# Kernel tuning notes

Measured on AMD Instinct MI355X. Metric: run time of the kernel, lower is better.

The kernel has to match this reference:

```python
import math
import jax, jax.numpy as jnp
import numpy as np

B, S, T, C, H = 4, 100, 128, 256, 256
NH, DH = 4, 32            # num_attention_heads//2, hidden_size//num_attention_heads
AH = NH * DH              # all_head_size = 128
FH = 32                   # fire_hidden_size
MAX_SP, MAX_TM, MAX_DOY = 180.0, 365.0, 182.0


def _fire(dist, c, w1, w2, max_dist):
    # FIREDistanceBias: log-compressed distance -> MLP(1->FH, SiLU, FH->1, no bias)
    c = jnp.maximum(c, 0.0)
    d = jnp.log(c * dist + 1.0) / jnp.log(c * max_dist + 1.0)
    h = jax.nn.silu(d[..., None] * w1[:, 0])   # (..., FH)
    return h @ w2[0]                            # (...,)


def setup_inputs() -> dict:
    key = jax.random.key(0)
    ks = jax.random.split(key, 20)
    p = 0.02
    inp = {
        "hidden_states": jax.random.normal(ks[0], (B, S, T, H), jnp.float32),
        "source_embeddings": jax.random.normal(ks[1], (B, S, C, H), jnp.float32),
        "attention_mask": jnp.zeros((B, 1, 1, T, C), jnp.float32),
        "st_dist": jax.random.uniform(ks[2], (B, T, C, 2), jnp.float32)
                   * jnp.array([MAX_SP, MAX_TM], jnp.float32),
        "st_doy_dist": jax.random.uniform(ks[3], (B, T, C), jnp.float32) * MAX_DOY,
        # attention projections (Linear H->AH with bias), output dense (AH->H)
        "Wq": jax.random.normal(ks[4], (AH, H), jnp.float32) * p,
        "bq": jnp.zeros((AH,), jnp.float32),
        "Wk": jax.random.normal(ks[5], (AH, H), jnp.float32) * p,
        "bk": jnp.zeros((AH,), jnp.float32),
        "Wv": jax.random.normal(ks[6], (AH, H), jnp.float32) * p,
        "bv": jnp.zeros((AH,), jnp.float32),
        "Wo": jax.random.normal(ks[7], (H, AH), jnp.float32) * p,
        "bo": jnp.zeros((H,), jnp.float32),
        # FIRE params: spatial / temporal / seasonal
        "c_s": jnp.float32(100.0),
        "w1_s": jax.random.normal(ks[8], (FH, 1), jnp.float32) * 0.5,
        "w2_s": jax.random.normal(ks[9], (1, FH), jnp.float32) * 0.5,
        "c_t": jnp.float32(100.0),
        "w1_t": jax.random.normal(ks[10], (FH, 1), jnp.float32) * 0.5,
        "w2_t": jax.random.normal(ks[11], (1, FH), jnp.float32) * 0.5,
        "c_d": jnp.float32(100.0),
        "w1_d": jax.random.normal(ks[12], (FH, 1), jnp.float32) * 0.5,
        "w2_d": jax.random.normal(ks[13], (1, FH), jnp.float32) * 0.5,
        # per-species log scales (init zeros in torch)
        "s_log_scale": jnp.zeros((S,), jnp.float32),
        "t_log_scale": jnp.zeros((S,), jnp.float32),
    }
    return inp


def reference(hidden_states, source_embeddings, attention_mask, st_dist, st_doy_dist,
              Wq, bq, Wk, bk, Wv, bv, Wo, bo,
              c_s, w1_s, w2_s, c_t, w1_t, w2_t, c_d, w1_d, w2_d,
              s_log_scale, t_log_scale):
    # FIRE distance biases over (B, T, C)
    sb = _fire(st_dist[..., 0], c_s, w1_s, w2_s, MAX_SP)
    tb = _fire(st_dist[..., 1], c_t, w1_t, w2_t, MAX_TM)
    db = _fire(st_doy_dist, c_d, w1_d, w2_d, MAX_DOY)
    # (B, S, T, C): species-scaled spatial+temporal + seasonal bias
    bias = (sb[:, None] * jnp.exp(s_log_scale)[None, :, None, None]
            + tb[:, None] * jnp.exp(t_log_scale)[None, :, None, None]
            + db[:, None])

    # projections; split heads: (B,S,L,AH) -> (B,S,NH,L,DH)
    q = (hidden_states @ Wq.T + bq).reshape(B, S, T, NH, DH).transpose(0, 1, 3, 2, 4)
    k = (source_embeddings @ Wk.T + bk).reshape(B, S, C, NH, DH).transpose(0, 1, 3, 2, 4)
    v = (source_embeddings @ Wv.T + bv).reshape(B, S, C, NH, DH).transpose(0, 1, 3, 2, 4)

    scores = jnp.einsum('bshtd,bshcd->bshtc', q, k) / math.sqrt(DH)
    scores = scores + attention_mask + bias[:, :, None]   # mask (B,1,1,T,C), bias (B,S,1,T,C)
    probs = jax.nn.softmax(scores, axis=-1)
    ctx = jnp.einsum('bshtc,bshcd->bshtd', probs, v)
    ctx = ctx.transpose(0, 1, 3, 2, 4).reshape(B, S, T, AH)
    return ctx @ Wo.T + bo   # STCrossOutput dense (dropout=0, eval)
```

## Files before the change

kernel.cpp:

```cpp
#include <hip/hip_runtime.h>
#include <hip/hip_bf16.h>
#include <math.h>

#define Bdim 4
#define Sdim 100
#define Tdim 128
#define Cdim 256
#define Hdim 256
#define NHd  4
#define DHd  32
#define AHd  128

typedef short bf16x8 __attribute__((ext_vector_type(8)));
typedef float f32x4 __attribute__((ext_vector_type(4)));

#define WAITCNT_V(n) do { \
  asm volatile("s_waitcnt vmcnt(" #n ")" ::: "memory"); \
  __builtin_amdgcn_sched_barrier(0); \
} while (0)

__device__ __forceinline__ short f2b(float x) {
  unsigned u = __float_as_uint(x);
  unsigned r = (u + 0x7FFF + ((u >> 16) & 1)) >> 16;
  return (short)r;
}

__device__ __forceinline__ void split2(float x, short& hi, short& lo) {
  unsigned u = __float_as_uint(x) & 0xFFFF0000u;
  hi = (short)(u >> 16);
  lo = f2b(x - __uint_as_float(u));
}

__device__ __forceinline__ float fire_eval(float dist, float c,
                                           const float* __restrict__ w1,
                                           const float* __restrict__ w2,
                                           float maxd) {
  c = fmaxf(c, 0.0f);
  float d = logf(fmaf(c, dist, 1.0f)) / logf(fmaf(c, maxd, 1.0f));
  float acc = 0.0f;
#pragma unroll
  for (int j = 0; j < 32; ++j) {
    float x = d * w1[j];
    float h = x / (1.0f + expf(-x));
    acc = fmaf(h, w2[j], acc);
  }
  return acc;
}

__global__ __launch_bounds__(256) void fire_bias_kernel(
    const float* __restrict__ st_dist, const float* __restrict__ st_doy,
    const float* __restrict__ mask,
    const float* __restrict__ c_s, const float* __restrict__ w1_s, const float* __restrict__ w2_s,
    const float* __restrict__ c_t, const float* __restrict__ w1_t, const float* __restrict__ w2_t,
    const float* __restrict__ c_d, const float* __restrict__ w1_d, const float* __restrict__ w2_d,
    float4* __restrict__ pk) {
  int i = blockIdx.x * 256 + threadIdx.x;
  if (i >= Bdim * Tdim * Cdim) return;
  float2 dv = ((const float2*)st_dist)[i];
  float4 r;
  r.x = fire_eval(dv.x, c_s[0], w1_s, w2_s, 180.0f);
  r.y = fire_eval(dv.y, c_t[0], w1_t, w2_t, 365.0f);
  r.z = fire_eval(st_doy[i], c_d[0], w1_d, w2_d, 182.0f) + mask[i];
  r.w = 0.0f;
  pk[i] = r;
}

__global__ __launch_bounds__(256) void bias_combine(
    const float4* __restrict__ pk,
    const float* __restrict__ sls, const float* __restrict__ tls,
    float* __restrict__ bC) {
  const int b = blockIdx.y;
  const int base = blockIdx.x * 1024 + threadIdx.x * 4;
  const float4* src = pk + (size_t)b * Tdim * Cdim + base;
  float sb[4], tb[4], db[4];
#pragma unroll
  for (int i = 0; i < 4; ++i) {
    float4 v = src[i];
    sb[i] = v.x; tb[i] = v.y; db[i] = v.z;
  }
  float* dst = bC + ((size_t)b * Sdim) * Tdim * Cdim + base;
  for (int s = 0; s < Sdim; ++s) {
    float es = __expf(sls[s]), et = __expf(tls[s]);
    float4 o;
    o.x = fmaf(sb[0], es, fmaf(tb[0], et, db[0]));
    o.y = fmaf(sb[1], es, fmaf(tb[1], et, db[1]));
    o.z = fmaf(sb[2], es, fmaf(tb[2], et, db[2]));
    o.w = fmaf(sb[3], es, fmaf(tb[3], et, db[3]));
    *(float4*)(dst + (size_t)s * Tdim * Cdim) = o;
  }
}

__global__ __launch_bounds__(256) void wsplit_pack(
    const float* __restrict__ Wq, const float* __restrict__ Wk,
    const float* __restrict__ Wv, const float* __restrict__ Wo,
    short* __restrict__ pack) {
  int which = blockIdx.y;
  const float* W = which == 0 ? Wq : which == 1 ? Wk : which == 2 ? Wv : Wo;
  int idx = blockIdx.x * 256 + threadIdx.x;
  int j = idx & 7;
  int l = (idx >> 3) & 63;
  int frag = idx >> 9;
  int nt, kk8, Kd;
  if (which == 3) { nt = frag & 15; kk8 = frag >> 4; Kd = 128; }
  else           { nt = frag & 7;  kk8 = frag >> 3; Kd = 256; }
  int n = nt * 16 + (l & 15);
  int k = kk8 * 32 + (l >> 4) * 8 + j;
  float val = W[(size_t)n * Kd + k];
  short h, lo_;
  if (which == 3) split2(val, h, lo_);
  else { h = f2b(val); lo_ = 0; }
  pack[(size_t)which * 65536 + idx] = h;
  pack[(size_t)which * 65536 + 32768 + idx] = lo_;
}


__global__ __launch_bounds__(512, 4) void proj_q_mfma(
    const float* __restrict__ A, const short* __restrict__ Wp,
    const float* __restrict__ bias, short* __restrict__ O, float scale) {
  __shared__ short wlds[2][8 * 512];
  const int tid = threadIdx.x;
  const int l = tid & 63, w = tid >> 6;
  const int lr = l & 15, lg = l >> 4;
  const int m0 = blockIdx.x * 128;
  const int arow = m0 + w * 16 + lr;
  const float* ap = A + (size_t)arow * 256 + lg * 8;

  auto stage = [&](int buf, int kk) {
    const short* gsrc = Wp + ((size_t)(kk * 8 + w) * 64 + l) * 8;
    int loff = __builtin_amdgcn_readfirstlane(buf * 4096 + w * 512);
    __builtin_amdgcn_global_load_lds(gsrc, &wlds[0][0] + loff, 16, 0, 0);
  };

  f32x4 acc[8] = {};
  stage(0, 0);
  float4 ca = *(const float4*)ap;
  float4 cb = *(const float4*)(ap + 4);
#pragma unroll
  for (int kk = 0; kk < 8; ++kk) {
    const int buf = kk & 1;
    float4 na, nb;
    if (kk < 7) {
      stage(buf ^ 1, kk + 1);
      const float* np = ap + (kk + 1) * 32;
      na = *(const float4*)np;
      nb = *(const float4*)(np + 4);
    }
    float av[8] = {ca.x, ca.y, ca.z, ca.w, cb.x, cb.y, cb.z, cb.w};
    bf16x8 af;
#pragma unroll
    for (int e = 0; e < 8; ++e) af[e] = f2b(av[e]);
    if (kk < 7) { WAITCNT_V(3); } else { WAITCNT_V(0); }
    __builtin_amdgcn_s_barrier();
    const short* lb = &wlds[0][0] + buf * 4096 + l * 8;
#pragma unroll
    for (int nt = 0; nt < 8; ++nt) {
      bf16x8 wv = *(const bf16x8*)(lb + nt * 512);
      acc[nt] = __builtin_amdgcn_mfma_f32_16x16x32_bf16(af, wv, acc[nt], 0, 0, 0);
    }
    __builtin_amdgcn_s_barrier();
    if (kk < 7) { ca = na; cb = nb; }
  }
#pragma unroll
  for (int nt = 0; nt < 8; ++nt)
#pragma unroll
    for (int r = 0; r < 4; ++r)
      O[(size_t)(m0 + w * 16 + lg * 4 + r) * 128 + nt * 16 + lr] =
          f2b((acc[nt][r] + bias[nt * 16 + lr]) * scale);
}

__global__ __launch_bounds__(512, 4) void proj_kv_mfma(
    const float* __restrict__ A,
    const short* __restrict__ Wkp, const float* __restrict__ bk,
    const short* __restrict__ Wvp, const float* __restrict__ bv,
    short* __restrict__ Ko, short* __restrict__ Vo) {
  __shared__ short wlds[2][16 * 512];
  const int tid = threadIdx.x;
  const int l = tid & 63, w = tid >> 6;
  const int lr = l & 15, lg = l >> 4;
  const int m0 = blockIdx.x * 128;
  const int arow = m0 + w * 16 + lr;
  const float* ap = A + (size_t)arow * 256 + lg * 8;

  auto stage = [&](int buf, int kk) {
#pragma unroll
    for (int r = 0; r < 2; ++r) {
      int f = w + 8 * r;
      const short* gsrc = (r ? Wvp : Wkp) + ((size_t)(kk * 8 + w) * 64 + l) * 8;
      int loff = __builtin_amdgcn_readfirstlane(buf * 8192 + f * 512);
      __builtin_amdgcn_global_load_lds(gsrc, &wlds[0][0] + loff, 16, 0, 0);
    }
  };

  f32x4 accK[8] = {}, accV[8] = {};
  stage(0, 0);
  float4 ca = *(const float4*)ap;
  float4 cb = *(const float4*)(ap + 4);
#pragma unroll
  for (int kk = 0; kk < 8; ++kk) {
    const int buf = kk & 1;
    float4 na, nb;
    if (kk < 7) {
      stage(buf ^ 1, kk + 1);
      const float* np = ap + (kk + 1) * 32;
      na = *(const float4*)np;
      nb = *(const float4*)(np + 4);
    }
    float av[8] = {ca.x, ca.y, ca.z, ca.w, cb.x, cb.y, cb.z, cb.w};
    bf16x8 af;
#pragma unroll
    for (int e = 0; e < 8; ++e) af[e] = f2b(av[e]);
    if (kk < 7) { WAITCNT_V(4); } else { WAITCNT_V(0); }
    __builtin_amdgcn_s_barrier();
    const short* lb = &wlds[0][0] + buf * 8192 + l * 8;
#pragma unroll
    for (int nt = 0; nt < 8; ++nt) {
      bf16x8 kw = *(const bf16x8*)(lb + nt * 512);
      bf16x8 vw = *(const bf16x8*)(lb + (8 + nt) * 512);
      accK[nt] = __builtin_amdgcn_mfma_f32_16x16x32_bf16(af, kw, accK[nt], 0, 0, 0);
      accV[nt] = __builtin_amdgcn_mfma_f32_16x16x32_bf16(af, vw, accV[nt], 0, 0, 0);
    }
    __builtin_amdgcn_s_barrier();
    if (kk < 7) { ca = na; cb = nb; }
  }
#pragma unroll
  for (int nt = 0; nt < 8; ++nt)
#pragma unroll
    for (int r = 0; r < 4; ++r) {
      size_t row = (size_t)(m0 + w * 16 + lg * 4 + r) * 128 + nt * 16 + lr;
      Ko[row] = f2b(accK[nt][r] + bk[nt * 16 + lr]);
      Vo[row] = f2b(accV[nt][r] + bv[nt * 16 + lr]);
    }
}

__global__ __launch_bounds__(512, 4) void proj_o_mfma(
    const short* __restrict__ Ahi, const short* __restrict__ Alo,
    const short* __restrict__ Wp, const float* __restrict__ bias,
    float* __restrict__ O) {
  __shared__ short wlds[2][32 * 512];
  const int tid = threadIdx.x;
  const int l = tid & 63, w = tid >> 6;
  const int lr = l & 15, lg = l >> 4;
  const int m0 = blockIdx.x * 128;
  const int arow = m0 + w * 16 + lr;
  const short* ah = Ahi + (size_t)arow * 128 + lg * 8;
  const short* al = Alo + (size_t)arow * 128 + lg * 8;

  auto stage = [&](int buf, int kk) {
#pragma unroll
    for (int r = 0; r < 4; ++r) {
      int f = w + 8 * r;
      const short* gsrc = Wp + ((f >> 4) ? 32768 : 0)
                          + ((size_t)(kk * 16 + (f & 15)) * 64 + l) * 8;
      int loff = __builtin_amdgcn_readfirstlane(buf * 16384 + f * 512);
      __builtin_amdgcn_global_load_lds(gsrc, &wlds[0][0] + loff, 16, 0, 0);
    }
  };

  f32x4 acc[16] = {};
  stage(0, 0);
  bf16x8 cah = *(const bf16x8*)ah;
  bf16x8 cal = *(const bf16x8*)al;
#pragma unroll
  for (int kk = 0; kk < 4; ++kk) {
    const int buf = kk & 1;
    bf16x8 nah, nal;
    if (kk < 3) {
      stage(buf ^ 1, kk + 1);
      nah = *(const bf16x8*)(ah + (kk + 1) * 32);
      nal = *(const bf16x8*)(al + (kk + 1) * 32);
    }
    if (kk < 3) { WAITCNT_V(6); } else { WAITCNT_V(0); }
    __builtin_amdgcn_s_barrier();
    const short* lb = &wlds[0][0] + buf * 16384 + l * 8;
#pragma unroll
    for (int nt = 0; nt < 16; ++nt) {
      bf16x8 whi = *(const bf16x8*)(lb + nt * 512);
      bf16x8 wlo = *(const bf16x8*)(lb + (16 + nt) * 512);
      acc[nt] = __builtin_amdgcn_mfma_f32_16x16x32_bf16(cah, whi, acc[nt], 0, 0, 0);
      acc[nt] = __builtin_amdgcn_mfma_f32_16x16x32_bf16(cah, wlo, acc[nt], 0, 0, 0);
      acc[nt] = __builtin_amdgcn_mfma_f32_16x16x32_bf16(cal, whi, acc[nt], 0, 0, 0);
    }
    __builtin_amdgcn_s_barrier();
    if (kk < 3) { cah = nah; cal = nal; }
  }
#pragma unroll
  for (int nt = 0; nt < 16; ++nt)
#pragma unroll
    for (int r = 0; r < 4; ++r)
      O[(size_t)(m0 + w * 16 + lg * 4 + r) * 256 + nt * 16 + lr] =
          acc[nt][r] + bias[nt * 16 + lr];
}

__global__ __launch_bounds__(512) void attn_mfma(
    const short* __restrict__ Qb, const short* __restrict__ Kb,
    const short* __restrict__ Vb,
    const float* __restrict__ bC,
    short* __restrict__ Chi, short* __restrict__ Clo) {
  __shared__ short vfrag[8][2][64][8];
  __shared__ short pbuf[8][16 * 36];

  const int tid = threadIdx.x;
  const int l = tid & 63;
  const int w = tid >> 6;
  const int lr = l & 15, lg = l >> 4;
  const int bid = blockIdx.x;
  const int xcd = bid & 7;
  const int i_  = bid >> 3;
  const int bs  = xcd * 50 + (i_ >> 2);
  const int h   = i_ & 3;

  const size_t kvbase = (size_t)bs * Cdim * AHd + h * DHd;
  const size_t qbase  = (size_t)bs * Tdim * AHd + h * DHd;

#pragma unroll
  for (int rep = 0; rep < 2; ++rep) {
    int chunk = tid * 2 + rep;
    int c = chunk >> 2, q = chunk & 3;
    bf16x8 v8 = *(const bf16x8*)(Vb + kvbase + (size_t)c * AHd + q * 8);
    int kc = c >> 5, nt = q >> 1;
    int lanebase = ((c & 31) >> 3) * 16 + (q & 1) * 8;
    int j = c & 7;
#pragma unroll
    for (int e = 0; e < 8; ++e)
      vfrag[kc][nt][lanebase + e][j] = v8[e];
  }
  __syncthreads();

  bf16x8 qf = *(const bf16x8*)(Qb + qbase + (size_t)(w * 16 + lr) * AHd + lg * 8);
  bf16x8 kf[16];
#pragma unroll
  for (int nt = 0; nt < 16; ++nt)
    kf[nt] = *(const bf16x8*)(Kb + kvbase + (size_t)(nt * 16 + lr) * AHd + lg * 8);

  const float* bb = bC + (size_t)bs * Tdim * Cdim + (size_t)(w * 16) * Cdim;
  f32x4 sacc[16];
#pragma unroll
  for (int nt = 0; nt < 16; ++nt) {
    f32x4 cinit;
#pragma unroll
    for (int r = 0; r < 4; ++r)
      cinit[r] = bb[(size_t)(lg * 4 + r) * Cdim + nt * 16 + lr];
    sacc[nt] = __builtin_amdgcn_mfma_f32_16x16x32_bf16(qf, kf[nt], cinit, 0, 0, 0);
  }

  float rinv[4];
#pragma unroll
  for (int nt = 0; nt < 16; ++nt)
#pragma unroll
    for (int r = 0; r < 4; ++r)
      sacc[nt][r] = __expf(sacc[nt][r]);
#pragma unroll
  for (int r = 0; r < 4; ++r) {
    float su = 0.f;
#pragma unroll
    for (int nt = 0; nt < 16; ++nt) su += sacc[nt][r];
#pragma unroll
    for (int off = 1; off < 16; off <<= 1) su += __shfl_xor(su, off);
    rinv[r] = 1.0f / su;
  }

  const f32x4 zero = {0.f, 0.f, 0.f, 0.f};
  f32x4 cacc[2] = {zero, zero};
  short* pb = &pbuf[w][0];
#pragma unroll
  for (int kc = 0; kc < 8; ++kc) {
#pragma unroll
    for (int ntl = 0; ntl < 2; ++ntl) {
      int nt = kc * 2 + ntl;
#pragma unroll
      for (int r = 0; r < 4; ++r)
        pb[(lg * 4 + r) * 36 + ntl * 16 + lr] = f2b(sacc[nt][r]);
    }
    bf16x8 af = *(const bf16x8*)&pb[lr * 36 + lg * 8];
#pragma unroll
    for (int ntd = 0; ntd < 2; ++ntd) {
      bf16x8 vf = *(const bf16x8*)&vfrag[kc][ntd][l][0];
      cacc[ntd] = __builtin_amdgcn_mfma_f32_16x16x32_bf16(af, vf, cacc[ntd], 0, 0, 0);
    }
  }

#pragma unroll
  for (int ntd = 0; ntd < 2; ++ntd)
#pragma unroll
    for (int r = 0; r < 4; ++r) {
      float val = cacc[ntd][r] * rinv[r];
      short h_, lo_;
      split2(val, h_, lo_);
      size_t idx = qbase + (size_t)(w * 16 + lg * 4 + r) * AHd + ntd * 16 + lr;
      Chi[idx] = h_;
      Clo[idx] = lo_;
    }
}

extern "C" void kernel_launch(void* const* d_in, const int* in_sizes, int n_in,
                              void* d_out, int out_size, void* d_ws, size_t ws_size,
                              hipStream_t stream) {
  const float* hs     = (const float*)d_in[0];
  const float* se     = (const float*)d_in[1];
  const float* mask   = (const float*)d_in[2];
  const float* stdist = (const float*)d_in[3];
  const float* stdoy  = (const float*)d_in[4];
  const float* Wq = (const float*)d_in[5];
  const float* bq = (const float*)d_in[6];
  const float* Wk = (const float*)d_in[7];
  const float* bk = (const float*)d_in[8];
  const float* Wv = (const float*)d_in[9];
  const float* bv = (const float*)d_in[10];
  const float* Wo = (const float*)d_in[11];
  const float* bo = (const float*)d_in[12];
  const float* c_s  = (const float*)d_in[13];
  const float* w1_s = (const float*)d_in[14];
  const float* w2_s = (const float*)d_in[15];
  const float* c_t  = (const float*)d_in[16];
  const float* w1_t = (const float*)d_in[17];
  const float* w2_t = (const float*)d_in[18];
  const float* c_d  = (const float*)d_in[19];
  const float* w1_d = (const float*)d_in[20];
  const float* w2_d = (const float*)d_in[21];
  const float* sls  = (const float*)d_in[22];
  const float* tls  = (const float*)d_in[23];
  float* out = (float*)d_out;

  float* ws = (float*)d_ws;
  const size_t BTC  = (size_t)Bdim * Tdim * Cdim;
  const size_t BSTC = (size_t)Bdim * Sdim * Tdim * Cdim;
  const size_t NQ   = (size_t)Bdim * Sdim * Tdim * AHd;
  const size_t NKV  = (size_t)Bdim * Sdim * Cdim * AHd;

  float4* pk  = (float4*)ws;
  float* bC   = ws + 4 * BTC;
  short* wpck = (short*)(bC + BSTC);
  short* Qb   = wpck + 262144;
  short* Kb   = Qb + NQ;
  short* Vb   = Kb + NKV;
  short* Chi  = Vb + NKV;
  short* Clo  = Chi + NQ;

  const int MQ  = Bdim * Sdim * Tdim;
  const int MKV = Bdim * Sdim * Cdim;

  fire_bias_kernel<<<(Bdim * Tdim * Cdim + 255) / 256, 256, 0, stream>>>(
      stdist, stdoy, mask, c_s, w1_s, w2_s, c_t, w1_t, w2_t, c_d, w1_d, w2_d, pk);

  bias_combine<<<dim3(Tdim * Cdim / 1024, Bdim), 256, 0, stream>>>(pk, sls, tls, bC);

  wsplit_pack<<<dim3(128, 4), 256, 0, stream>>>(Wq, Wk, Wv, Wo, wpck);

  proj_q_mfma<<<dim3(MQ / 128), 512, 0, stream>>>(hs, wpck, bq, Qb,
                                                  0.17677669529663687f);
  proj_kv_mfma<<<dim3(MKV / 128), 512, 0, stream>>>(
      se, wpck + 65536, bk, wpck + 131072, bv, Kb, Vb);

  attn_mfma<<<dim3(Bdim * Sdim * NHd), 512, 0, stream>>>(
      Qb, Kb, Vb, bC, Chi, Clo);

  proj_o_mfma<<<dim3(MQ / 128), 512, 0, stream>>>(Chi, Clo, wpck + 196608, bo, out);
}
```

Before: 162.4 us.

## Split attention T rows across two blocks and stream scores per K chunk

The attention kernel now launches twice as many 256-thread blocks, each handling half of the 128 query rows for one (b,s,head). K fragments, bias loads, exp and row-sum accumulation move inside the kc loop, so the 16-entry score and K register arrays are no longer held, which cuts register pressure and raises the occupancy hint. The cost is that V staging into LDS is repeated by both blocks that share a head, and the K loads are now interleaved with compute instead of issued all at once up front.

```diff
diff --git a/kernel.cpp b/kernel.cpp
--- a/kernel.cpp
+++ b/kernel.cpp
@@ -291,13 +291,13 @@
           acc[nt][r] + bias[nt * 16 + lr];
 }
 
-__global__ __launch_bounds__(512) void attn_mfma(
+__global__ __launch_bounds__(256, 6) void attn_mfma(
     const short* __restrict__ Qb, const short* __restrict__ Kb,
     const short* __restrict__ Vb,
     const float* __restrict__ bC,
     short* __restrict__ Chi, short* __restrict__ Clo) {
   __shared__ short vfrag[8][2][64][8];
-  __shared__ short pbuf[8][16 * 36];
+  __shared__ short pbuf[4][16 * 36];
 
   const int tid = threadIdx.x;
   const int l = tid & 63;
@@ -306,70 +306,53 @@
   const int bid = blockIdx.x;
   const int xcd = bid & 7;
   const int i_  = bid >> 3;
-  const int bs  = xcd * 50 + (i_ >> 2);
-  const int h   = i_ & 3;
+  const int bs  = xcd * 50 + (i_ >> 3);
+  const int rem = i_ & 7;
+  const int h   = rem >> 1;
+  const int th  = rem & 1;
 
   const size_t kvbase = (size_t)bs * Cdim * AHd + h * DHd;
   const size_t qbase  = (size_t)bs * Tdim * AHd + h * DHd;
-
-#pragma unroll
-  for (int rep = 0; rep < 2; ++rep) {
-    int chunk = tid * 2 + rep;
-    int c = chunk >> 2, q = chunk & 3;
+  const int trow0 = th * 64 + w * 16;
+
+#pragma unroll
+  for (int q = 0; q < 4; ++q) {
+    int c = tid;
     bf16x8 v8 = *(const bf16x8*)(Vb + kvbase + (size_t)c * AHd + q * 8);
-    int kc = c >> 5, nt = q >> 1;
+    int kc = c >> 5, ntd = q >> 1;
     int lanebase = ((c & 31) >> 3) * 16 + (q & 1) * 8;
     int j = c & 7;
 #pragma unroll
     for (int e = 0; e < 8; ++e)
-      vfrag[kc][nt][lanebase + e][j] = v8[e];
+      vfrag[kc][ntd][lanebase + e][j] = v8[e];
   }
   __syncthreads();
 
-  bf16x8 qf = *(const bf16x8*)(Qb + qbase + (size_t)(w * 16 + lr) * AHd + lg * 8);
-  bf16x8 kf[16];
-#pragma unroll
-  for (int nt = 0; nt < 16; ++nt)
-    kf[nt] = *(const bf16x8*)(Kb + kvbase + (size_t)(nt * 16 + lr) * AHd + lg * 8);
-
-  const float* bb = bC + (size_t)bs * Tdim * Cdim + (size_t)(w * 16) * Cdim;
-  f32x4 sacc[16];
-#pragma unroll
-  for (int nt = 0; nt < 16; ++nt) {
-    f32x4 cinit;
-#pragma unroll
-    for (int r = 0; r < 4; ++r)
-      cinit[r] = bb[(size_t)(lg * 4 + r) * Cdim + nt * 16 + lr];
-    sacc[nt] = __builtin_amdgcn_mfma_f32_16x16x32_bf16(qf, kf[nt], cinit, 0, 0, 0);
-  }
-
-  float rinv[4];
-#pragma unroll
-  for (int nt = 0; nt < 16; ++nt)
-#pragma unroll
-    for (int r = 0; r < 4; ++r)
-      sacc[nt][r] = __expf(sacc[nt][r]);
-#pragma unroll
-  for (int r = 0; r < 4; ++r) {
-    float su = 0.f;
-#pragma unroll
-    for (int nt = 0; nt < 16; ++nt) su += sacc[nt][r];
-#pragma unroll
-    for (int off = 1; off < 16; off <<= 1) su += __shfl_xor(su, off);
-    rinv[r] = 1.0f / su;
-  }
+  bf16x8 qf = *(const bf16x8*)(Qb + qbase + (size_t)(trow0 + lr) * AHd + lg * 8);
+  const float* bb = bC + (size_t)bs * Tdim * Cdim + (size_t)trow0 * Cdim;
 
   const f32x4 zero = {0.f, 0.f, 0.f, 0.f};
   f32x4 cacc[2] = {zero, zero};
+  float su[4] = {0.f, 0.f, 0.f, 0.f};
   short* pb = &pbuf[w][0];
+
 #pragma unroll
   for (int kc = 0; kc < 8; ++kc) {
 #pragma unroll
     for (int ntl = 0; ntl < 2; ++ntl) {
-      int nt = kc * 2 + ntl;
+      const int nt = kc * 2 + ntl;
+      bf16x8 kf = *(const bf16x8*)(Kb + kvbase + (size_t)(nt * 16 + lr) * AHd + lg * 8);
+      f32x4 cinit;
 #pragma unroll
       for (int r = 0; r < 4; ++r)
-        pb[(lg * 4 + r) * 36 + ntl * 16 + lr] = f2b(sacc[nt][r]);
+        cinit[r] = bb[(size_t)(lg * 4 + r) * Cdim + nt * 16 + lr];
+      f32x4 s = __builtin_amdgcn_mfma_f32_16x16x32_bf16(qf, kf, cinit, 0, 0, 0);
+#pragma unroll
+      for (int r = 0; r < 4; ++r) {
+        float e = __expf(s[r]);
+        su[r] += e;
+        pb[(lg * 4 + r) * 36 + ntl * 16 + lr] = f2b(e);
+      }
     }
     bf16x8 af = *(const bf16x8*)&pb[lr * 36 + lg * 8];
 #pragma unroll
@@ -377,6 +360,15 @@
       bf16x8 vf = *(const bf16x8*)&vfrag[kc][ntd][l][0];
       cacc[ntd] = __builtin_amdgcn_mfma_f32_16x16x32_bf16(af, vf, cacc[ntd], 0, 0, 0);
     }
+  }
+
+  float rinv[4];
+#pragma unroll
+  for (int r = 0; r < 4; ++r) {
+    float s = su[r];
+#pragma unroll
+    for (int off = 1; off < 16; off <<= 1) s += __shfl_xor(s, off);
+    rinv[r] = 1.0f / s;
   }
 
 #pragma unroll
@@ -386,7 +378,7 @@
       float val = cacc[ntd][r] * rinv[r];
       short h_, lo_;
       split2(val, h_, lo_);
-      size_t idx = qbase + (size_t)(w * 16 + lg * 4 + r) * AHd + ntd * 16 + lr;
+      size_t idx = qbase + (size_t)(trow0 + lg * 4 + r) * AHd + ntd * 16 + lr;
       Chi[idx] = h_;
       Clo[idx] = lo_;
     }
@@ -451,7 +443,7 @@
   proj_kv_mfma<<<dim3(MKV / 128), 512, 0, stream>>>(
       se, wpck + 65536, bk, wpck + 131072, bv, Kb, Vb);
 
-  attn_mfma<<<dim3(Bdim * Sdim * NHd), 512, 0, stream>>>(
+  attn_mfma<<<dim3(Bdim * Sdim * NHd * 2), 256, 0, stream>>>(
       Qb, Kb, Vb, bC, Chi, Clo);
 
   proj_o_mfma<<<dim3(MQ / 128), 512, 0, stream>>>(Chi, Clo, wpck + 196608, bo, out);
```

Measured after the change: 165.2 us. About the same (+1.7%).

## Store bias in MFMA fragment order and swizzle V LDS rows

Applied to the files above, without the earlier changes.

The combined bias tensor is now written by bias_combine directly in the per-lane MFMA accumulator layout, so attention loads each tile's four init values with one float4 instead of four strided scalar loads. The V fragment array in LDS gets an XOR row permutation on both write and read to reduce bank conflicts. attn_mfma also gets a minimum-occupancy launch bound of 2. The bias producer grid changes to match the new layout, and its write pattern and the register-budget limit are possible costs.

```diff
diff --git a/kernel.cpp b/kernel.cpp
--- a/kernel.cpp
+++ b/kernel.cpp
@@ -68,17 +68,19 @@
 __global__ __launch_bounds__(256) void bias_combine(
     const float4* __restrict__ pk,
     const float* __restrict__ sls, const float* __restrict__ tls,
-    float* __restrict__ bC) {
-  const int b = blockIdx.y;
-  const int base = blockIdx.x * 1024 + threadIdx.x * 4;
-  const float4* src = pk + (size_t)b * Tdim * Cdim + base;
+    float* __restrict__ bF) {
+  const int l = threadIdx.x & 63;
+  const int lr = l & 15, lg = l >> 4;
+  const int nt = blockIdx.x * 4 + (threadIdx.x >> 6);
+  const int wt = blockIdx.y;
+  const int b  = blockIdx.z;
+  const int c = nt * 16 + lr;
   float sb[4], tb[4], db[4];
 #pragma unroll
-  for (int i = 0; i < 4; ++i) {
-    float4 v = src[i];
-    sb[i] = v.x; tb[i] = v.y; db[i] = v.z;
-  }
-  float* dst = bC + ((size_t)b * Sdim) * Tdim * Cdim + base;
+  for (int r = 0; r < 4; ++r) {
+    float4 v = pk[(size_t)b * Tdim * Cdim + (size_t)(wt * 16 + lg * 4 + r) * Cdim + c];
+    sb[r] = v.x; tb[r] = v.y; db[r] = v.z;
+  }
   for (int s = 0; s < Sdim; ++s) {
     float es = __expf(sls[s]), et = __expf(tls[s]);
     float4 o;
@@ -86,7 +88,8 @@
     o.y = fmaf(sb[1], es, fmaf(tb[1], et, db[1]));
     o.z = fmaf(sb[2], es, fmaf(tb[2], et, db[2]));
     o.w = fmaf(sb[3], es, fmaf(tb[3], et, db[3]));
-    *(float4*)(dst + (size_t)s * Tdim * Cdim) = o;
+    size_t idx = ((((size_t)(b * Sdim + s) * 8 + wt) * 16 + nt) * 64 + l);
+    *(float4*)(bF + idx * 4) = o;
   }
 }
 
@@ -113,7 +116,6 @@
   pack[(size_t)which * 65536 + 32768 + idx] = lo_;
 }
 
-
 __global__ __launch_bounds__(512, 4) void proj_q_mfma(
     const float* __restrict__ A, const short* __restrict__ Wp,
     const float* __restrict__ bias, short* __restrict__ O, float scale) {
@@ -291,10 +293,10 @@
           acc[nt][r] + bias[nt * 16 + lr];
 }
 
-__global__ __launch_bounds__(512) void attn_mfma(
+__global__ __launch_bounds__(512, 2) void attn_mfma(
     const short* __restrict__ Qb, const short* __restrict__ Kb,
     const short* __restrict__ Vb,
-    const float* __restrict__ bC,
+    const float* __restrict__ bF,
     short* __restrict__ Chi, short* __restrict__ Clo) {
   __shared__ short vfrag[8][2][64][8];
   __shared__ short pbuf[8][16 * 36];
@@ -321,8 +323,11 @@
     int lanebase = ((c & 31) >> 3) * 16 + (q & 1) * 8;
     int j = c & 7;
 #pragma unroll
-    for (int e = 0; e < 8; ++e)
-      vfrag[kc][nt][lanebase + e][j] = v8[e];
+    for (int e = 0; e < 8; ++e) {
+      int row = lanebase + e;
+      int prow = row ^ ((row >> 4) << 1);
+      vfrag[kc][nt][prow][j] = v8[e];
+    }
   }
   __syncthreads();
 
@@ -332,14 +337,12 @@
   for (int nt = 0; nt < 16; ++nt)
     kf[nt] = *(const bf16x8*)(Kb + kvbase + (size_t)(nt * 16 + lr) * AHd + lg * 8);
 
-  const float* bb = bC + (size_t)bs * Tdim * Cdim + (size_t)(w * 16) * Cdim;
+  const float4* bb = (const float4*)bF + ((size_t)bs * 8 + w) * 16 * 64 + l;
   f32x4 sacc[16];
 #pragma unroll
   for (int nt = 0; nt < 16; ++nt) {
-    f32x4 cinit;
-#pragma unroll
-    for (int r = 0; r < 4; ++r)
-      cinit[r] = bb[(size_t)(lg * 4 + r) * Cdim + nt * 16 + lr];
+    float4 cv = bb[nt * 64];
+    f32x4 cinit = {cv.x, cv.y, cv.z, cv.w};
     sacc[nt] = __builtin_amdgcn_mfma_f32_16x16x32_bf16(qf, kf[nt], cinit, 0, 0, 0);
   }
 
@@ -362,6 +365,7 @@
   const f32x4 zero = {0.f, 0.f, 0.f, 0.f};
   f32x4 cacc[2] = {zero, zero};
   short* pb = &pbuf[w][0];
+  const int lp = l ^ ((l >> 4) << 1);
 #pragma unroll
   for (int kc = 0; kc < 8; ++kc) {
 #pragma unroll
@@ -374,7 +378,7 @@
     bf16x8 af = *(const bf16x8*)&pb[lr * 36 + lg * 8];
 #pragma unroll
     for (int ntd = 0; ntd < 2; ++ntd) {
-      bf16x8 vf = *(const bf16x8*)&vfrag[kc][ntd][l][0];
+      bf16x8 vf = *(const bf16x8*)&vfrag[kc][ntd][lp][0];
       cacc[ntd] = __builtin_amdgcn_mfma_f32_16x16x32_bf16(af, vf, cacc[ntd], 0, 0, 0);
     }
   }
@@ -428,8 +432,8 @@
   const size_t NKV  = (size_t)Bdim * Sdim * Cdim * AHd;
 
   float4* pk  = (float4*)ws;
-  float* bC   = ws + 4 * BTC;
-  short* wpck = (short*)(bC + BSTC);
+  float* bF   = ws + 4 * BTC;
+  short* wpck = (short*)(bF + BSTC);
   short* Qb   = wpck + 262144;
   short* Kb   = Qb + NQ;
   short* Vb   = Kb + NKV;
@@ -442,7 +446,7 @@
   fire_bias_kernel<<<(Bdim * Tdim * Cdim + 255) / 256, 256, 0, stream>>>(
       stdist, stdoy, mask, c_s, w1_s, w2_s, c_t, w1_t, w2_t, c_d, w1_d, w2_d, pk);
 
-  bias_combine<<<dim3(Tdim * Cdim / 1024, Bdim), 256, 0, stream>>>(pk, sls, tls, bC);
+  bias_combine<<<dim3(4, 8, Bdim), 256, 0, stream>>>(pk, sls, tls, bF);
 
   wsplit_pack<<<dim3(128, 4), 256, 0, stream>>>(Wq, Wk, Wv, Wo, wpck);
 
@@ -452,7 +456,7 @@
       se, wpck + 65536, bk, wpck + 131072, bv, Kb, Vb);
 
   attn_mfma<<<dim3(Bdim * Sdim * NHd), 512, 0, stream>>>(
-      Qb, Kb, Vb, bC, Chi, Clo);
+      Qb, Kb, Vb, bF, Chi, Clo);
 
   proj_o_mfma<<<dim3(MQ / 128), 512, 0, stream>>>(Chi, Clo, wpck + 196608, bo, out);
 }
```

After: 162.4 us. About the same (-0.0%).
